# Optimization experiments

Measured on AMD Instinct MI355X. Metric: run time of the kernel, lower is better.

The kernel has to match this reference:

```python
import jax, jax.numpy as jnp
import numpy as np

B, N, D, H = 2, 512, 384, 12
SQK, SV, PQ, PV = 16, 16, 4, 8
SCALE = 1.0 / np.sqrt(SQK + 4 * PQ)  # attention_scale, point_pair_dim=4
EPS = 1e-12


def setup_inputs() -> dict:
    key = jax.random.key(0)
    ks = jax.random.split(key, 10)

    def w(k, fan_in, fan_out):
        return (jax.random.normal(k, (fan_in, fan_out), jnp.float32) / np.sqrt(fan_in))

    return {
        "hidden": jax.random.normal(ks[0], (B, N, D), jnp.float32),
        "xyz": jax.random.normal(ks[1], (B, N, 3), jnp.float32),
        "W_qk": w(ks[2], D, 2 * H * SQK), "b_qk": jnp.zeros((2 * H * SQK,), jnp.float32),
        "W_vs": w(ks[3], D, H * SV), "b_vs": jnp.zeros((H * SV,), jnp.float32),
        "W_so": w(ks[4], H * SV, D), "b_so": jnp.zeros((D,), jnp.float32),
        "W_pqk": w(ks[5], D, H * PQ * 3), "b_pqk": jnp.zeros((H * PQ * 3,), jnp.float32),
        "W_pv": w(ks[6], D, H * PV * 3), "b_pv": jnp.zeros((H * PV * 3,), jnp.float32),
        "W_po": w(ks[7], H * PV * 3, D), "b_po": jnp.zeros((D,), jnp.float32),
        "W_fp": w(ks[8], 2 * D, D), "b_fp": jnp.zeros((D,), jnp.float32),
    }


def reference(hidden, xyz, W_qk, b_qk, W_vs, b_vs, W_so, b_so,
              W_pqk, b_pqk, W_pv, b_pv, W_po, b_po, W_fp, b_fp):
    # scalar q/k/v (note: heads are NOT split in the attention matmuls, per source)
    qk = hidden @ W_qk + b_qk                       # [B,N,2*H*SQK]
    q_s, k_s = jnp.split(qk, 2, axis=-1)            # [B,N,H*SQK] each
    v_s = hidden @ W_vs + b_vs                      # [B,N,H*SV]

    # points; k_points = q_points in source
    qp = (hidden @ W_pqk + b_pqk).reshape(B, N, H, PQ, 3)
    vp = hidden @ W_pv + b_pv                       # [B,N,H*PV*3]

    scalar_attn = jnp.einsum('bid,bjd->bij', q_s, k_s)  # [B,N,N]

    # fused pairwise point features: dist(q_i, k_j) + sum of 3 cosine components
    # = dist + cos_sim, per (head, point); avoid materializing [B,N,N,H,P,3].
    dot = jnp.einsum('bihpc,bjhpc->bijhp', qp, qp)      # [B,N,N,H,PQ]
    n2 = jnp.sum(qp * qp, axis=-1)                      # [B,N,H,PQ]
    d2 = n2[:, :, None] + n2[:, None] - 2.0 * dot
    dist = jnp.sqrt(jnp.maximum(d2, 0.0) + EPS)
    nrm = jnp.sqrt(n2 + EPS)
    cos = dot / (nrm[:, :, None] * nrm[:, None])
    point_attn = jnp.sum(dist + cos, axis=(-1, -2))     # [B,N,N]

    attn = jax.nn.softmax((scalar_attn + point_attn) * SCALE, axis=-1)

    scalar_result = jnp.einsum('bij,bjd->bid', attn, v_s)   # [B,N,H*SV]
    point_result = jnp.einsum('bij,bjd->bid', attn, vp)     # [B,N,H*PV*3]

    scalar_result = scalar_result @ W_so + b_so             # [B,N,D]
    point_result = point_result @ W_po + b_po               # [B,N,D]

    result = jnp.concatenate([scalar_result, point_result], axis=-1) @ W_fp + b_fp
    delta_xyz = point_result.reshape(B, N, -1, 3).mean(axis=2)  # [B,N,3]
    return result, xyz + delta_xyz
```

## Files before the change

kernel.cpp:

```cpp
#include <hip/hip_runtime.h>
#include <math.h>

typedef unsigned short u16;
typedef __attribute__((ext_vector_type(8))) short bf16x8;
typedef __attribute__((ext_vector_type(4))) float f32x4;

#define BB 2
#define NN 512
#define SCALEF 0.17677669529663687f

__device__ __forceinline__ u16 f2bf(float x) {
  union { float f; unsigned u; } c; c.f = x;
  unsigned r = (c.u + 0x7FFFu + ((c.u >> 16) & 1u)) >> 16;
  return (u16)r;
}
__device__ __forceinline__ float bf2f(u16 h) {
  union { unsigned u; float f; } c; c.u = ((unsigned)h) << 16;
  return c.f;
}
__device__ __forceinline__ void pack8(const float* v, bf16x8& h, bf16x8& l) {
#pragma unroll
  for (int j = 0; j < 8; ++j) {
    u16 hi = f2bf(v[j]);
    h[j] = (short)hi;
    l[j] = (short)f2bf(v[j] - bf2f(hi));
  }
}
#define MFMA3(ACC, AH, AL, BH, BL)                                              \
  ACC = __builtin_amdgcn_mfma_f32_16x16x32_bf16(AH, BH, ACC, 0, 0, 0);          \
  ACC = __builtin_amdgcn_mfma_f32_16x16x32_bf16(AH, BL, ACC, 0, 0, 0);          \
  ACC = __builtin_amdgcn_mfma_f32_16x16x32_bf16(AL, BH, ACC, 0, 0, 0);

template<int MR, int NF>
__device__ __forceinline__ void mfma_tile(
    const u16* __restrict__ Ah, const u16* __restrict__ Al, int lda,
    const u16* __restrict__ Bh, const u16* __restrict__ Bl, int ldb,
    int kBeg, int kEnd, int arow, int bcol, f32x4 (&acc)[MR][NF]) {
  const int lane = threadIdx.x & 63;
  const int rr = lane & 15, kg = lane >> 4;
  const u16* pah = Ah + (size_t)(arow + rr) * lda + kg * 8;
  const u16* pal = Al + (size_t)(arow + rr) * lda + kg * 8;
  const u16* pbh = Bh + (size_t)(bcol + rr) * ldb + kg * 8;
  const u16* pbl = Bl + (size_t)(bcol + rr) * ldb + kg * 8;
#pragma unroll 2
  for (int k0 = kBeg; k0 < kEnd; k0 += 32) {
    bf16x8 a_h[MR], a_l[MR], b_h[NF], b_l[NF];
#pragma unroll
    for (int m = 0; m < MR; ++m) {
      a_h[m] = *(const bf16x8*)(pah + (size_t)m * 16 * lda + k0);
      a_l[m] = *(const bf16x8*)(pal + (size_t)m * 16 * lda + k0);
    }
#pragma unroll
    for (int f = 0; f < NF; ++f) {
      b_h[f] = *(const bf16x8*)(pbh + (size_t)f * 16 * ldb + k0);
      b_l[f] = *(const bf16x8*)(pbl + (size_t)f * 16 * ldb + k0);
    }
#pragma unroll
    for (int m = 0; m < MR; ++m)
#pragma unroll
      for (int f = 0; f < NF; ++f) { MFMA3(acc[m][f], a_h[m], a_l[m], b_h[f], b_l[f]) }
  }
}

__global__ __launch_bounds__(256) void k_input(
    const float* __restrict__ hidden, const float* __restrict__ xyz,
    const float* __restrict__ W_qk, const float* __restrict__ b_qk,
    const float* __restrict__ W_vs, const float* __restrict__ b_vs,
    const float* __restrict__ W_pv, const float* __restrict__ b_pv,
    const float* __restrict__ W_pqk, const float* __restrict__ b_pqk,
    u16* __restrict__ QKh, u16* __restrict__ QKl,
    u16* __restrict__ VTh, u16* __restrict__ VTl,
    float* __restrict__ QPf, float* __restrict__ out_xyz) {
  __shared__ f32x4 CB[3][2][3][64];
  __shared__ u16 Dh[48][32], Dl[48][32];
  const int tid = threadIdx.x;
  const int w = tid >> 6, lane = tid & 63;
  const int rr = lane & 15, kg = lane >> 4;
  const int row0 = blockIdx.y * 32, col0 = blockIdx.x * 48;

  if (blockIdx.x == 18) {
    for (int t2 = tid; t2 < 96; t2 += 256)
      out_xyz[(size_t)row0 * 3 + t2] = xyz[(size_t)row0 * 3 + t2];
  }

  const float* W; const float* bias; int Ns, region;
  if (col0 < 384)      { W = W_qk;  Ns = 384; bias = b_qk + col0;          W += col0;       region = 0; }
  else if (col0 < 576) { W = W_vs;  Ns = 192; bias = b_vs + (col0 - 384);  W += col0 - 384; region = 1; }
  else if (col0 < 864) { W = W_pv;  Ns = 288; bias = b_pv + (col0 - 576);  W += col0 - 576; region = 1; }
  else                 { W = W_pqk; Ns = 144; bias = b_pqk + (col0 - 864); W += col0 - 864; region = 2; }

  f32x4 acc[2][3] = {};
  const float* pa = hidden + (size_t)(row0 + rr) * 384 + kg * 8;
  const float* pw = W + rr;
  for (int k0 = w * 32; k0 < 384; k0 += 128) {
    bf16x8 a_h[2], a_l[2], b_h[3], b_l[3];
#pragma unroll
    for (int m = 0; m < 2; ++m) {
      float v[8];
      *(float4*)&v[0] = *(const float4*)(pa + (size_t)m * 16 * 384 + k0);
      *(float4*)&v[4] = *(const float4*)(pa + (size_t)m * 16 * 384 + k0 + 4);
      pack8(v, a_h[m], a_l[m]);
    }
    const float* bp0 = pw + (size_t)(k0 + kg * 8) * Ns;
#pragma unroll
    for (int f = 0; f < 3; ++f) {
      float v[8];
#pragma unroll
      for (int j = 0; j < 8; ++j) v[j] = bp0[(size_t)j * Ns + f * 16];
      pack8(v, b_h[f], b_l[f]);
    }
#pragma unroll
    for (int m = 0; m < 2; ++m)
#pragma unroll
      for (int f = 0; f < 3; ++f) { MFMA3(acc[m][f], a_h[m], a_l[m], b_h[f], b_l[f]) }
  }
  if (w) {
#pragma unroll
    for (int m = 0; m < 2; ++m)
#pragma unroll
      for (int f = 0; f < 3; ++f) CB[w - 1][m][f][lane] = acc[m][f];
  }
  __syncthreads();
  if (w) return;
#pragma unroll
  for (int wv = 0; wv < 3; ++wv)
#pragma unroll
    for (int m = 0; m < 2; ++m)
#pragma unroll
      for (int f = 0; f < 3; ++f) acc[m][f] += CB[wv][m][f][lane];

  const int rb = (lane >> 4) << 2, cc = lane & 15;
  if (region == 0) {
#pragma unroll
    for (int f = 0; f < 3; ++f) {
      int n = col0 + f * 16 + cc;
      float bv = bias[f * 16 + cc];
#pragma unroll
      for (int m = 0; m < 2; ++m)
#pragma unroll
        for (int r = 0; r < 4; ++r) {
          float v = acc[m][f][r] + bv;
          int row = row0 + m * 16 + rb + r;
          u16 hi = f2bf(v);
          QKh[(size_t)row * 384 + n] = hi;
          QKl[(size_t)row * 384 + n] = f2bf(v - bf2f(hi));
        }
    }
  } else if (region == 2) {
#pragma unroll
    for (int f = 0; f < 3; ++f) {
      int c = (col0 - 864) + f * 16 + cc;
      float bv = bias[f * 16 + cc];
#pragma unroll
      for (int m = 0; m < 2; ++m)
#pragma unroll
        for (int r = 0; r < 4; ++r)
          QPf[(size_t)(row0 + m * 16 + rb + r) * 144 + c] = acc[m][f][r] + bv;
    }
  } else {
#pragma unroll
    for (int f = 0; f < 3; ++f) {
      float bv = bias[f * 16 + cc];
#pragma unroll
      for (int m = 0; m < 2; ++m)
#pragma unroll
        for (int r = 0; r < 4; ++r) {
          float v = acc[m][f][r] + bv;
          u16 hi = f2bf(v);
          Dh[f * 16 + cc][m * 16 + rb + r] = hi;
          Dl[f * 16 + cc][m * 16 + rb + r] = f2bf(v - bf2f(hi));
        }
    }
    const int b = row0 >> 9, rl = row0 & 511;
    const int cbase = col0 - 384;
    u16* dsth = VTh + (size_t)b * 480 * 512;
    u16* dstl = VTl + (size_t)b * 480 * 512;
    for (int u = lane; u < 192; u += 64) {
      int c = u >> 2, seg = u & 3;
      *(uint4*)(dsth + (size_t)(cbase + c) * 512 + rl + seg * 8) = *(const uint4*)&Dh[c][seg * 8];
      *(uint4*)(dstl + (size_t)(cbase + c) * 512 + rl + seg * 8) = *(const uint4*)&Dl[c][seg * 8];
    }
  }
}

#define PROW 244
__global__ __launch_bounds__(256) void k_attn(
    const u16* __restrict__ QKh, const u16* __restrict__ QKl,
    const float* __restrict__ QPf, float* __restrict__ ATTf) {
  __shared__ float Pi[32][PROW];
  __shared__ float Pj[32][PROW];
  __shared__ float Sf[32 * 33];
  const int b = blockIdx.z;
  int t = blockIdx.x, ti_ = 0;
  while (t >= 16 - ti_) { t -= 16 - ti_; ++ti_; }
  const int tj_ = ti_ + t;
  const int i0 = ti_ * 32, j0 = tj_ * 32;
  const bool offdiag = (tj_ != ti_);
  const int tid = threadIdx.x;
  for (int u = tid; u < 3072; u += 256) {
    int side = (u >= 1536) ? 1 : 0;
    int rem = u - side * 1536;
    int row = rem / 48, hp = rem - row * 48;
    int grow = b * NN + (side ? j0 : i0) + row;
    const float* p = QPf + (size_t)grow * 144 + hp * 3;
    float x = p[0], y = p[1], z = p[2];
    float n2 = x * x + y * y + z * z;
    float inv = __frsqrt_rn(n2 + 1e-12f);
    float* dst = side ? &Pj[row][0] : &Pi[row][0];
    ((float4*)dst)[hp] = make_float4(x, y, z, n2);
    dst[192 + hp] = inv;
  }
  __syncthreads();
  const int tj = tid & 15, ti = tid >> 4;
  float a00 = 0.f, a01 = 0.f, a10 = 0.f, a11 = 0.f;
  {
    const float4* A0 = (const float4*)&Pi[ti][0];
    const float4* A1 = (const float4*)&Pi[ti + 16][0];
    const float4* B0 = (const float4*)&Pj[tj][0];
    const float4* B1 = (const float4*)&Pj[tj + 16][0];
    const float* iA0 = &Pi[ti][192];
    const float* iA1 = &Pi[ti + 16][192];
    const float* iB0 = &Pj[tj][192];
    const float* iB1 = &Pj[tj + 16][192];
#pragma unroll 4
    for (int hp = 0; hp < 48; ++hp) {
      float4 p0 = A0[hp], p1 = A1[hp], q0 = B0[hp], q1 = B1[hp];
      float va0 = iA0[hp], va1 = iA1[hp], vb0 = iB0[hp], vb1 = iB1[hp];
      {
        float dot = p0.x * q0.x + p0.y * q0.y + p0.z * q0.z;
        float d2 = fmaxf(fmaf(-2.f, dot, p0.w + q0.w), 0.f) + 1e-12f;
        a00 += d2 * __frsqrt_rn(d2) + dot * (va0 * vb0);
      }
      {
        float dot = p0.x * q1.x + p0.y * q1.y + p0.z * q1.z;
        float d2 = fmaxf(fmaf(-2.f, dot, p0.w + q1.w), 0.f) + 1e-12f;
        a01 += d2 * __frsqrt_rn(d2) + dot * (va0 * vb1);
      }
      {
        float dot = p1.x * q0.x + p1.y * q0.y + p1.z * q0.z;
        float d2 = fmaxf(fmaf(-2.f, dot, p1.w + q0.w), 0.f) + 1e-12f;
        a10 += d2 * __frsqrt_rn(d2) + dot * (va1 * vb0);
      }
      {
        float dot = p1.x * q1.x + p1.y * q1.y + p1.z * q1.z;
        float d2 = fmaxf(fmaf(-2.f, dot, p1.w + q1.w), 0.f) + 1e-12f;
        a11 += d2 * __frsqrt_rn(d2) + dot * (va1 * vb1);
      }
    }
  }
  Sf[ti * 33 + tj] = a00;
  Sf[ti * 33 + tj + 16] = a01;
  Sf[(ti + 16) * 33 + tj] = a10;
  Sf[(ti + 16) * 33 + tj + 16] = a11;
  f32x4 qij[1][1] = {}, qji[1][1] = {};
  const int w = tid >> 6, lane = tid & 63;
  {
    int arow = b * NN + i0 + (w >> 1) * 16;
    int brow = b * NN + j0 + (w & 1) * 16;
    mfma_tile<1, 1>(QKh, QKl, 384, QKh + 192, QKl + 192, 384, 0, 192, arow, brow, qij);
    if (offdiag) {
      int arow2 = b * NN + j0 + (w >> 1) * 16;
      int brow2 = b * NN + i0 + (w & 1) * 16;
      mfma_tile<1, 1>(QKh, QKl, 384, QKh + 192, QKl + 192, 384, 0, 192, arow2, brow2, qji);
    }
  }
  __syncthreads();
  const int rl = (w >> 1) * 16 + ((lane >> 4) << 2);
  const int cl = (w & 1) * 16 + (lane & 15);
  float* Cb = ATTf + (size_t)b * NN * NN;
#pragma unroll
  for (int r = 0; r < 4; ++r)
    Cb[(size_t)(i0 + rl + r) * NN + j0 + cl] = qij[0][0][r] + Sf[(rl + r) * 33 + cl];
  if (offdiag) {
#pragma unroll
    for (int r = 0; r < 4; ++r)
      Cb[(size_t)(j0 + rl + r) * NN + i0 + cl] = qji[0][0][r] + Sf[cl * 33 + rl + r];
  }
}

__global__ __launch_bounds__(256) void k_pv(
    const float* __restrict__ ATTf,
    const u16* __restrict__ VTh, const u16* __restrict__ VTl,
    u16* __restrict__ SRh, u16* __restrict__ SRl) {
  __shared__ f32x4 CB[3][2][3][64];
  __shared__ float RS[3][2][64];
  const int tid = threadIdx.x;
  const int w = tid >> 6, lane = tid & 63;
  const int rr = lane & 15, kg = lane >> 4;
  const int b = blockIdx.z;
  const int row0 = blockIdx.y * 32, col0 = blockIdx.x * 48;
  const float* pa = ATTf + (size_t)(b * NN + row0 + rr) * NN + kg * 8;
  const u16* pbh = VTh + (size_t)b * 480 * 512 + (size_t)(col0 + rr) * 512 + kg * 8;
  const u16* pbl = VTl + (size_t)b * 480 * 512 + (size_t)(col0 + rr) * 512 + kg * 8;
  f32x4 acc[2][3] = {};
  float rs0 = 0.f, rs1 = 0.f;
  for (int k0 = w * 32; k0 < NN; k0 += 128) {
    bf16x8 a_h[2], a_l[2], b_h[3], b_l[3];
#pragma unroll
    for (int m = 0; m < 2; ++m) {
      float v[8];
      *(float4*)&v[0] = *(const float4*)(pa + (size_t)m * 16 * NN + k0);
      *(float4*)&v[4] = *(const float4*)(pa + (size_t)m * 16 * NN + k0 + 4);
      float part = 0.f;
#pragma unroll
      for (int j = 0; j < 8; ++j) { float e = __expf(v[j] * SCALEF); part += e; v[j] = e; }
      if (m == 0) rs0 += part; else rs1 += part;
      pack8(v, a_h[m], a_l[m]);
    }
#pragma unroll
    for (int f = 0; f < 3; ++f) {
      b_h[f] = *(const bf16x8*)(pbh + (size_t)f * 16 * 512 + k0);
      b_l[f] = *(const bf16x8*)(pbl + (size_t)f * 16 * 512 + k0);
    }
#pragma unroll
    for (int m = 0; m < 2; ++m)
#pragma unroll
      for (int f = 0; f < 3; ++f) { MFMA3(acc[m][f], (m ? a_h[1] : a_h[0]), (m ? a_l[1] : a_l[0]), b_h[f], b_l[f]) }
  }
  if (w) {
#pragma unroll
    for (int m = 0; m < 2; ++m)
#pragma unroll
      for (int f = 0; f < 3; ++f) CB[w - 1][m][f][lane] = acc[m][f];
    RS[w - 1][0][lane] = rs0;
    RS[w - 1][1][lane] = rs1;
  }
  __syncthreads();
  if (w) return;
#pragma unroll
  for (int wv = 0; wv < 3; ++wv) {
#pragma unroll
    for (int m = 0; m < 2; ++m)
#pragma unroll
      for (int f = 0; f < 3; ++f) acc[m][f] += CB[wv][m][f][lane];
    rs0 += RS[wv][0][lane];
    rs1 += RS[wv][1][lane];
  }
  rs0 += __shfl_xor(rs0, 16); rs0 += __shfl_xor(rs0, 32);
  rs1 += __shfl_xor(rs1, 16); rs1 += __shfl_xor(rs1, 32);
  const int rb = (lane >> 4) << 2, cc = lane & 15;
  float inv0[4], inv1[4];
#pragma unroll
  for (int r = 0; r < 4; ++r) {
    inv0[r] = 1.0f / __shfl(rs0, rb + r);
    inv1[r] = 1.0f / __shfl(rs1, rb + r);
  }
  u16* oh = SRh + (size_t)b * NN * 480;
  u16* ol = SRl + (size_t)b * NN * 480;
#pragma unroll
  for (int m = 0; m < 2; ++m)
#pragma unroll
    for (int f = 0; f < 3; ++f) {
      int n = col0 + f * 16 + cc;
#pragma unroll
      for (int r = 0; r < 4; ++r) {
        float v = acc[m][f][r] * (m ? inv1[r] : inv0[r]);
        u16 hi = f2bf(v);
        oh[(size_t)(row0 + m * 16 + rb + r) * 480 + n] = hi;
        ol[(size_t)(row0 + m * 16 + rb + r) * 480 + n] = f2bf(v - bf2f(hi));
      }
    }
}

__global__ __launch_bounds__(256) void k_outproj(
    const u16* __restrict__ SRh, const u16* __restrict__ SRl,
    const float* __restrict__ W_so, const float* __restrict__ b_so,
    const float* __restrict__ W_po, const float* __restrict__ b_po,
    u16* __restrict__ PRh, u16* __restrict__ PRl, float* __restrict__ out_xyz) {
  __shared__ f32x4 CB[3][2][3][64];
  __shared__ float D[32][49];
  const int tid = threadIdx.x;
  const int w = tid >> 6, lane = tid & 63;
  const int rr = lane & 15, kg = lane >> 4;
  const int t = blockIdx.x;
  const int row0 = blockIdx.y * 32, col0 = t * 48;
  const float* W = (t < 8) ? W_so : W_po;
  const int kBeg = (t < 8) ? 0 : 192, kEnd = (t < 8) ? 192 : 480;
  const int wcol = (t < 8) ? col0 : col0 - 384;
  const u16* pah = SRh + (size_t)(row0 + rr) * 480 + kg * 8;
  const u16* pal = SRl + (size_t)(row0 + rr) * 480 + kg * 8;
  const float* pw = W + wcol + rr;
  f32x4 acc[2][3] = {};
  for (int k0 = kBeg + w * 32; k0 < kEnd; k0 += 128) {
    bf16x8 a_h[2], a_l[2], b_h[3], b_l[3];
#pragma unroll
    for (int m = 0; m < 2; ++m) {
      a_h[m] = *(const bf16x8*)(pah + (size_t)m * 16 * 480 + k0);
      a_l[m] = *(const bf16x8*)(pal + (size_t)m * 16 * 480 + k0);
    }
    const float* bp0 = pw + (size_t)(k0 - kBeg + kg * 8) * 384;
#pragma unroll
    for (int f = 0; f < 3; ++f) {
      float v[8];
#pragma unroll
      for (int j = 0; j < 8; ++j) v[j] = bp0[(size_t)j * 384 + f * 16];
      pack8(v, b_h[f], b_l[f]);
    }
#pragma unroll
    for (int m = 0; m < 2; ++m)
#pragma unroll
      for (int f = 0; f < 3; ++f) { MFMA3(acc[m][f], a_h[m], a_l[m], b_h[f], b_l[f]) }
  }
  if (w) {
#pragma unroll
    for (int m = 0; m < 2; ++m)
#pragma unroll
      for (int f = 0; f < 3; ++f) CB[w - 1][m][f][lane] = acc[m][f];
  }
  __syncthreads();
  if (w) return;
#pragma unroll
  for (int wv = 0; wv < 3; ++wv)
#pragma unroll
    for (int m = 0; m < 2; ++m)
#pragma unroll
      for (int f = 0; f < 3; ++f) acc[m][f] += CB[wv][m][f][lane];
  const int rb = (lane >> 4) << 2, cc = lane & 15;
#pragma unroll
  for (int m = 0; m < 2; ++m)
#pragma unroll
    for (int f = 0; f < 3; ++f) {
      int n = col0 + f * 16 + cc;
      float bias = (n < 384) ? b_so[n] : b_po[n - 384];
#pragma unroll
      for (int r = 0; r < 4; ++r) {
        float v = acc[m][f][r] + bias;
        u16 hi = f2bf(v);
        PRh[(size_t)(row0 + m * 16 + rb + r) * 768 + n] = hi;
        PRl[(size_t)(row0 + m * 16 + rb + r) * 768 + n] = f2bf(v - bf2f(hi));
        if (t >= 8) D[m * 16 + rb + r][f * 16 + cc] = v;
      }
    }
  if (t >= 8) {
    if (lane < 32) {
      float sx = 0.f, sy = 0.f, sz = 0.f;
#pragma unroll
      for (int p = 0; p < 16; ++p) {
        sx += D[lane][3 * p];
        sy += D[lane][3 * p + 1];
        sz += D[lane][3 * p + 2];
      }
      int token = row0 + lane;
      atomicAdd(out_xyz + (size_t)token * 3 + 0, sx * (1.0f / 128.f));
      atomicAdd(out_xyz + (size_t)token * 3 + 1, sy * (1.0f / 128.f));
      atomicAdd(out_xyz + (size_t)token * 3 + 2, sz * (1.0f / 128.f));
    }
  }
}

__global__ __launch_bounds__(256) void k_final(
    const u16* __restrict__ PRh, const u16* __restrict__ PRl,
    const float* __restrict__ W_fp, const float* __restrict__ b_fp,
    float* __restrict__ out_res) {
  __shared__ f32x4 CB[3][2][3][64];
  const int tid = threadIdx.x;
  const int w = tid >> 6, lane = tid & 63;
  const int rr = lane & 15, kg = lane >> 4;
  const int row0 = blockIdx.y * 32, col0 = blockIdx.x * 48;
  const u16* pah = PRh + (size_t)(row0 + rr) * 768 + kg * 8;
  const u16* pal = PRl + (size_t)(row0 + rr) * 768 + kg * 8;
  const float* pw = W_fp + col0 + rr;
  f32x4 acc[2][3] = {};
  for (int k0 = w * 32; k0 < 768; k0 += 128) {
    bf16x8 a_h[2], a_l[2], b_h[3], b_l[3];
#pragma unroll
    for (int m = 0; m < 2; ++m) {
      a_h[m] = *(const bf16x8*)(pah + (size_t)m * 16 * 768 + k0);
      a_l[m] = *(const bf16x8*)(pal + (size_t)m * 16 * 768 + k0);
    }
    const float* bp0 = pw + (size_t)(k0 + kg * 8) * 384;
#pragma unroll
    for (int f = 0; f < 3; ++f) {
      float v[8];
#pragma unroll
      for (int j = 0; j < 8; ++j) v[j] = bp0[(size_t)j * 384 + f * 16];
      pack8(v, b_h[f], b_l[f]);
    }
#pragma unroll
    for (int m = 0; m < 2; ++m)
#pragma unroll
      for (int f = 0; f < 3; ++f) { MFMA3(acc[m][f], a_h[m], a_l[m], b_h[f], b_l[f]) }
  }
  if (w) {
#pragma unroll
    for (int m = 0; m < 2; ++m)
#pragma unroll
      for (int f = 0; f < 3; ++f) CB[w - 1][m][f][lane] = acc[m][f];
  }
  __syncthreads();
  if (w) return;
#pragma unroll
  for (int wv = 0; wv < 3; ++wv)
#pragma unroll
    for (int m = 0; m < 2; ++m)
#pragma unroll
      for (int f = 0; f < 3; ++f) acc[m][f] += CB[wv][m][f][lane];
  const int rb = (lane >> 4) << 2, cc = lane & 15;
#pragma unroll
  for (int m = 0; m < 2; ++m)
#pragma unroll
    for (int f = 0; f < 3; ++f) {
      int n = col0 + f * 16 + cc;
#pragma unroll
      for (int r = 0; r < 4; ++r)
        out_res[(size_t)(row0 + m * 16 + rb + r) * 384 + n] = acc[m][f][r] + b_fp[n];
    }
}

extern "C" void kernel_launch(void* const* d_in, const int* in_sizes, int n_in,
                              void* d_out, int out_size, void* d_ws, size_t ws_size,
                              hipStream_t stream) {
  const float* hidden = (const float*)d_in[0];
  const float* xyz   = (const float*)d_in[1];
  const float* W_qk  = (const float*)d_in[2];
  const float* b_qk  = (const float*)d_in[3];
  const float* W_vs  = (const float*)d_in[4];
  const float* b_vs  = (const float*)d_in[5];
  const float* W_so  = (const float*)d_in[6];
  const float* b_so  = (const float*)d_in[7];
  const float* W_pqk = (const float*)d_in[8];
  const float* b_pqk = (const float*)d_in[9];
  const float* W_pv  = (const float*)d_in[10];
  const float* b_pv  = (const float*)d_in[11];
  const float* W_po  = (const float*)d_in[12];
  const float* b_po  = (const float*)d_in[13];
  const float* W_fp  = (const float*)d_in[14];
  const float* b_fp  = (const float*)d_in[15];

  float* out_res = (float*)d_out;
  float* out_xyz = out_res + (size_t)BB * NN * 384;

  u16* p   = (u16*)d_ws;
  u16* QKh = p;            p += 393216;
  u16* QKl = p;            p += 393216;
  u16* VTh = p;            p += 491520;
  u16* VTl = p;            p += 491520;
  u16* SRh = p;            p += 491520;
  u16* SRl = p;            p += 491520;
  u16* PRh = p;            p += 786432;
  u16* PRl = p;            p += 786432;
  float* QPf  = (float*)p; p += 2 * 147456;
  float* ATTf = (float*)p;

  k_input<<<dim3(21, 32), 256, 0, stream>>>(hidden, xyz,
                                            W_qk, b_qk, W_vs, b_vs, W_pv, b_pv, W_pqk, b_pqk,
                                            QKh, QKl, VTh, VTl, QPf, out_xyz);
  k_attn<<<dim3(136, 1, 2), 256, 0, stream>>>(QKh, QKl, QPf, ATTf);
  k_pv<<<dim3(10, 16, 2), 256, 0, stream>>>(ATTf, VTh, VTl, SRh, SRl);
  k_outproj<<<dim3(16, 32), 256, 0, stream>>>(SRh, SRl, W_so, b_so, W_po, b_po,
                                              PRh, PRl, out_xyz);
  k_final<<<dim3(8, 32), 256, 0, stream>>>(PRh, PRl, W_fp, b_fp, out_res);
}
```

Baseline: 73.98 us.

## Double threads per block and split K/head work across more waves in all kernels

Every kernel moves from 256 to 512 threads. k_input and the GEMM-style kernels split the K reduction over 8 waves instead of 4, with a wider shared-memory cross-wave reduction. k_pv, k_outproj and k_final also halve the row tile to 16, doubling the grid. k_attn splits the 48 head-point loop across two 256-thread halves and gives the two transposed scalar MFMA tiles to separate waves. The aim is more parallelism and latency hiding in these small, latency-bound kernels, at the cost of more reduction traffic, more blocks, and less reuse of the B operand per block.

```diff
diff --git a/kernel.cpp b/kernel.cpp
--- a/kernel.cpp
+++ b/kernel.cpp
@@ -62,7 +62,7 @@
   }
 }
 
-__global__ __launch_bounds__(256) void k_input(
+__global__ __launch_bounds__(512) void k_input(
     const float* __restrict__ hidden, const float* __restrict__ xyz,
     const float* __restrict__ W_qk, const float* __restrict__ b_qk,
     const float* __restrict__ W_vs, const float* __restrict__ b_vs,
@@ -71,7 +71,7 @@
     u16* __restrict__ QKh, u16* __restrict__ QKl,
     u16* __restrict__ VTh, u16* __restrict__ VTl,
     float* __restrict__ QPf, float* __restrict__ out_xyz) {
-  __shared__ f32x4 CB[3][2][3][64];
+  __shared__ f32x4 CB[7][2][3][64];
   __shared__ u16 Dh[48][32], Dl[48][32];
   const int tid = threadIdx.x;
   const int w = tid >> 6, lane = tid & 63;
@@ -79,7 +79,7 @@
   const int row0 = blockIdx.y * 32, col0 = blockIdx.x * 48;
 
   if (blockIdx.x == 18) {
-    for (int t2 = tid; t2 < 96; t2 += 256)
+    for (int t2 = tid; t2 < 96; t2 += 512)
       out_xyz[(size_t)row0 * 3 + t2] = xyz[(size_t)row0 * 3 + t2];
   }
 
@@ -92,7 +92,7 @@
   f32x4 acc[2][3] = {};
   const float* pa = hidden + (size_t)(row0 + rr) * 384 + kg * 8;
   const float* pw = W + rr;
-  for (int k0 = w * 32; k0 < 384; k0 += 128) {
+  for (int k0 = w * 32; k0 < 384; k0 += 256) {
     bf16x8 a_h[2], a_l[2], b_h[3], b_l[3];
 #pragma unroll
     for (int m = 0; m < 2; ++m) {
@@ -123,7 +123,7 @@
   __syncthreads();
   if (w) return;
 #pragma unroll
-  for (int wv = 0; wv < 3; ++wv)
+  for (int wv = 0; wv < 7; ++wv)
 #pragma unroll
     for (int m = 0; m < 2; ++m)
 #pragma unroll
@@ -184,12 +184,12 @@
 }
 
 #define PROW 244
-__global__ __launch_bounds__(256) void k_attn(
+__global__ __launch_bounds__(512) void k_attn(
     const u16* __restrict__ QKh, const u16* __restrict__ QKl,
     const float* __restrict__ QPf, float* __restrict__ ATTf) {
   __shared__ float Pi[32][PROW];
   __shared__ float Pj[32][PROW];
-  __shared__ float Sf[32 * 33];
+  __shared__ float Sf[2][32 * 33];
   const int b = blockIdx.z;
   int t = blockIdx.x, ti_ = 0;
   while (t >= 16 - ti_) { t -= 16 - ti_; ++ti_; }
@@ -197,7 +197,7 @@
   const int i0 = ti_ * 32, j0 = tj_ * 32;
   const bool offdiag = (tj_ != ti_);
   const int tid = threadIdx.x;
-  for (int u = tid; u < 3072; u += 256) {
+  for (int u = tid; u < 3072; u += 512) {
     int side = (u >= 1536) ? 1 : 0;
     int rem = u - side * 1536;
     int row = rem / 48, hp = rem - row * 48;
@@ -211,9 +211,11 @@
     dst[192 + hp] = inv;
   }
   __syncthreads();
-  const int tj = tid & 15, ti = tid >> 4;
-  float a00 = 0.f, a01 = 0.f, a10 = 0.f, a11 = 0.f;
+  const int h = tid >> 8;
+  const int t8 = tid & 255;
+  const int tj = t8 & 15, ti = t8 >> 4;
   {
+    float a00 = 0.f, a01 = 0.f, a10 = 0.f, a11 = 0.f;
     const float4* A0 = (const float4*)&Pi[ti][0];
     const float4* A1 = (const float4*)&Pi[ti + 16][0];
     const float4* B0 = (const float4*)&Pj[tj][0];
@@ -222,8 +224,9 @@
     const float* iA1 = &Pi[ti + 16][192];
     const float* iB0 = &Pj[tj][192];
     const float* iB1 = &Pj[tj + 16][192];
+    const int hpB = h * 24, hpE = hpB + 24;
 #pragma unroll 4
-    for (int hp = 0; hp < 48; ++hp) {
+    for (int hp = hpB; hp < hpE; ++hp) {
       float4 p0 = A0[hp], p1 = A1[hp], q0 = B0[hp], q1 = B1[hp];
       float va0 = iA0[hp], va1 = iA1[hp], vb0 = iB0[hp], vb1 = iB1[hp];
       {
@@ -247,65 +250,65 @@
         a11 += d2 * __frsqrt_rn(d2) + dot * (va1 * vb1);
       }
     }
-  }
-  Sf[ti * 33 + tj] = a00;
-  Sf[ti * 33 + tj + 16] = a01;
-  Sf[(ti + 16) * 33 + tj] = a10;
-  Sf[(ti + 16) * 33 + tj + 16] = a11;
-  f32x4 qij[1][1] = {}, qji[1][1] = {};
+    Sf[h][ti * 33 + tj] = a00;
+    Sf[h][ti * 33 + tj + 16] = a01;
+    Sf[h][(ti + 16) * 33 + tj] = a10;
+    Sf[h][(ti + 16) * 33 + tj + 16] = a11;
+  }
   const int w = tid >> 6, lane = tid & 63;
-  {
-    int arow = b * NN + i0 + (w >> 1) * 16;
-    int brow = b * NN + j0 + (w & 1) * 16;
-    mfma_tile<1, 1>(QKh, QKl, 384, QKh + 192, QKl + 192, 384, 0, 192, arow, brow, qij);
-    if (offdiag) {
-      int arow2 = b * NN + j0 + (w >> 1) * 16;
-      int brow2 = b * NN + i0 + (w & 1) * 16;
-      mfma_tile<1, 1>(QKh, QKl, 384, QKh + 192, QKl + 192, 384, 0, 192, arow2, brow2, qji);
-    }
+  const int dir = w >> 2, sub = w & 3;
+  f32x4 q[1][1] = {};
+  if (dir == 0) {
+    int arow = b * NN + i0 + (sub >> 1) * 16;
+    int brow = b * NN + j0 + (sub & 1) * 16;
+    mfma_tile<1, 1>(QKh, QKl, 384, QKh + 192, QKl + 192, 384, 0, 192, arow, brow, q);
+  } else if (offdiag) {
+    int arow = b * NN + j0 + (sub >> 1) * 16;
+    int brow = b * NN + i0 + (sub & 1) * 16;
+    mfma_tile<1, 1>(QKh, QKl, 384, QKh + 192, QKl + 192, 384, 0, 192, arow, brow, q);
   }
   __syncthreads();
-  const int rl = (w >> 1) * 16 + ((lane >> 4) << 2);
-  const int cl = (w & 1) * 16 + (lane & 15);
+  const int rl = (sub >> 1) * 16 + ((lane >> 4) << 2);
+  const int cl = (sub & 1) * 16 + (lane & 15);
   float* Cb = ATTf + (size_t)b * NN * NN;
-#pragma unroll
-  for (int r = 0; r < 4; ++r)
-    Cb[(size_t)(i0 + rl + r) * NN + j0 + cl] = qij[0][0][r] + Sf[(rl + r) * 33 + cl];
-  if (offdiag) {
+  if (dir == 0) {
 #pragma unroll
     for (int r = 0; r < 4; ++r)
-      Cb[(size_t)(j0 + rl + r) * NN + i0 + cl] = qji[0][0][r] + Sf[cl * 33 + rl + r];
-  }
-}
-
-__global__ __launch_bounds__(256) void k_pv(
+      Cb[(size_t)(i0 + rl + r) * NN + j0 + cl] =
+          q[0][0][r] + Sf[0][(rl + r) * 33 + cl] + Sf[1][(rl + r) * 33 + cl];
+  } else if (offdiag) {
+#pragma unroll
+    for (int r = 0; r < 4; ++r)
+      Cb[(size_t)(j0 + rl + r) * NN + i0 + cl] =
+          q[0][0][r] + Sf[0][cl * 33 + rl + r] + Sf[1][cl * 33 + rl + r];
+  }
+}
+
+__global__ __launch_bounds__(512) void k_pv(
     const float* __restrict__ ATTf,
     const u16* __restrict__ VTh, const u16* __restrict__ VTl,
     u16* __restrict__ SRh, u16* __restrict__ SRl) {
-  __shared__ f32x4 CB[3][2][3][64];
-  __shared__ float RS[3][2][64];
+  __shared__ f32x4 CB[7][3][64];
+  __shared__ float RS[7][64];
   const int tid = threadIdx.x;
   const int w = tid >> 6, lane = tid & 63;
   const int rr = lane & 15, kg = lane >> 4;
   const int b = blockIdx.z;
-  const int row0 = blockIdx.y * 32, col0 = blockIdx.x * 48;
+  const int row0 = blockIdx.y * 16, col0 = blockIdx.x * 48;
   const float* pa = ATTf + (size_t)(b * NN + row0 + rr) * NN + kg * 8;
   const u16* pbh = VTh + (size_t)b * 480 * 512 + (size_t)(col0 + rr) * 512 + kg * 8;
   const u16* pbl = VTl + (size_t)b * 480 * 512 + (size_t)(col0 + rr) * 512 + kg * 8;
-  f32x4 acc[2][3] = {};
-  float rs0 = 0.f, rs1 = 0.f;
-  for (int k0 = w * 32; k0 < NN; k0 += 128) {
-    bf16x8 a_h[2], a_l[2], b_h[3], b_l[3];
-#pragma unroll
-    for (int m = 0; m < 2; ++m) {
+  f32x4 acc[3] = {};
+  float rs = 0.f;
+  for (int k0 = w * 32; k0 < NN; k0 += 256) {
+    bf16x8 a_h, a_l, b_h[3], b_l[3];
+    {
       float v[8];
-      *(float4*)&v[0] = *(const float4*)(pa + (size_t)m * 16 * NN + k0);
-      *(float4*)&v[4] = *(const float4*)(pa + (size_t)m * 16 * NN + k0 + 4);
-      float part = 0.f;
-#pragma unroll
-      for (int j = 0; j < 8; ++j) { float e = __expf(v[j] * SCALEF); part += e; v[j] = e; }
-      if (m == 0) rs0 += part; else rs1 += part;
-      pack8(v, a_h[m], a_l[m]);
+      *(float4*)&v[0] = *(const float4*)(pa + k0);
+      *(float4*)&v[4] = *(const float4*)(pa + k0 + 4);
+#pragma unroll
+      for (int j = 0; j < 8; ++j) { float e = __expf(v[j] * SCALEF); rs += e; v[j] = e; }
+      pack8(v, a_h, a_l);
     }
 #pragma unroll
     for (int f = 0; f < 3; ++f) {
@@ -313,81 +316,65 @@
       b_l[f] = *(const bf16x8*)(pbl + (size_t)f * 16 * 512 + k0);
     }
 #pragma unroll
-    for (int m = 0; m < 2; ++m)
-#pragma unroll
-      for (int f = 0; f < 3; ++f) { MFMA3(acc[m][f], (m ? a_h[1] : a_h[0]), (m ? a_l[1] : a_l[0]), b_h[f], b_l[f]) }
+    for (int f = 0; f < 3; ++f) { MFMA3(acc[f], a_h, a_l, b_h[f], b_l[f]) }
   }
   if (w) {
 #pragma unroll
-    for (int m = 0; m < 2; ++m)
-#pragma unroll
-      for (int f = 0; f < 3; ++f) CB[w - 1][m][f][lane] = acc[m][f];
-    RS[w - 1][0][lane] = rs0;
-    RS[w - 1][1][lane] = rs1;
+    for (int f = 0; f < 3; ++f) CB[w - 1][f][lane] = acc[f];
+    RS[w - 1][lane] = rs;
   }
   __syncthreads();
   if (w) return;
 #pragma unroll
-  for (int wv = 0; wv < 3; ++wv) {
-#pragma unroll
-    for (int m = 0; m < 2; ++m)
-#pragma unroll
-      for (int f = 0; f < 3; ++f) acc[m][f] += CB[wv][m][f][lane];
-    rs0 += RS[wv][0][lane];
-    rs1 += RS[wv][1][lane];
-  }
-  rs0 += __shfl_xor(rs0, 16); rs0 += __shfl_xor(rs0, 32);
-  rs1 += __shfl_xor(rs1, 16); rs1 += __shfl_xor(rs1, 32);
+  for (int wv = 0; wv < 7; ++wv) {
+#pragma unroll
+    for (int f = 0; f < 3; ++f) acc[f] += CB[wv][f][lane];
+    rs += RS[wv][lane];
+  }
+  rs += __shfl_xor(rs, 16);
+  rs += __shfl_xor(rs, 32);
   const int rb = (lane >> 4) << 2, cc = lane & 15;
-  float inv0[4], inv1[4];
-#pragma unroll
-  for (int r = 0; r < 4; ++r) {
-    inv0[r] = 1.0f / __shfl(rs0, rb + r);
-    inv1[r] = 1.0f / __shfl(rs1, rb + r);
-  }
+  float inv[4];
+#pragma unroll
+  for (int r = 0; r < 4; ++r) inv[r] = 1.0f / __shfl(rs, rb + r);
   u16* oh = SRh + (size_t)b * NN * 480;
   u16* ol = SRl + (size_t)b * NN * 480;
 #pragma unroll
-  for (int m = 0; m < 2; ++m)
-#pragma unroll
-    for (int f = 0; f < 3; ++f) {
-      int n = col0 + f * 16 + cc;
-#pragma unroll
-      for (int r = 0; r < 4; ++r) {
-        float v = acc[m][f][r] * (m ? inv1[r] : inv0[r]);
-        u16 hi = f2bf(v);
-        oh[(size_t)(row0 + m * 16 + rb + r) * 480 + n] = hi;
-        ol[(size_t)(row0 + m * 16 + rb + r) * 480 + n] = f2bf(v - bf2f(hi));
-      }
-    }
-}
-
-__global__ __launch_bounds__(256) void k_outproj(
+  for (int f = 0; f < 3; ++f) {
+    int n = col0 + f * 16 + cc;
+#pragma unroll
+    for (int r = 0; r < 4; ++r) {
+      float v = acc[f][r] * inv[r];
+      u16 hi = f2bf(v);
+      oh[(size_t)(row0 + rb + r) * 480 + n] = hi;
+      ol[(size_t)(row0 + rb + r) * 480 + n] = f2bf(v - bf2f(hi));
+    }
+  }
+}
+
+__global__ __launch_bounds__(512) void k_outproj(
     const u16* __restrict__ SRh, const u16* __restrict__ SRl,
     const float* __restrict__ W_so, const float* __restrict__ b_so,
     const float* __restrict__ W_po, const float* __restrict__ b_po,
     u16* __restrict__ PRh, u16* __restrict__ PRl, float* __restrict__ out_xyz) {
-  __shared__ f32x4 CB[3][2][3][64];
-  __shared__ float D[32][49];
+  __shared__ f32x4 CB[7][3][64];
+  __shared__ float D[16][49];
   const int tid = threadIdx.x;
   const int w = tid >> 6, lane = tid & 63;
   const int rr = lane & 15, kg = lane >> 4;
   const int t = blockIdx.x;
-  const int row0 = blockIdx.y * 32, col0 = t * 48;
+  const int row0 = blockIdx.y * 16, col0 = t * 48;
   const float* W = (t < 8) ? W_so : W_po;
   const int kBeg = (t < 8) ? 0 : 192, kEnd = (t < 8) ? 192 : 480;
   const int wcol = (t < 8) ? col0 : col0 - 384;
   const u16* pah = SRh + (size_t)(row0 + rr) * 480 + kg * 8;
   const u16* pal = SRl + (size_t)(row0 + rr) * 480 + kg * 8;
   const float* pw = W + wcol + rr;
-  f32x4 acc[2][3] = {};
-  for (int k0 = kBeg + w * 32; k0 < kEnd; k0 += 128) {
-    bf16x8 a_h[2], a_l[2], b_h[3], b_l[3];
-#pragma unroll
-    for (int m = 0; m < 2; ++m) {
-      a_h[m] = *(const bf16x8*)(pah + (size_t)m * 16 * 480 + k0);
-      a_l[m] = *(const bf16x8*)(pal + (size_t)m * 16 * 480 + k0);
-    }
+  f32x4 acc[3] = {};
+  for (int k0 = kBeg + w * 32; k0 < kEnd; k0 += 256) {
+    bf16x8 a_h, a_l, b_h[3], b_l[3];
+    a_h = *(const bf16x8*)(pah + k0);
+    a_l = *(const bf16x8*)(pal + k0);
     const float* bp0 = pw + (size_t)(k0 - kBeg + kg * 8) * 384;
 #pragma unroll
     for (int f = 0; f < 3; ++f) {
@@ -397,77 +384,64 @@
       pack8(v, b_h[f], b_l[f]);
     }
 #pragma unroll
-    for (int m = 0; m < 2; ++m)
-#pragma unroll
-      for (int f = 0; f < 3; ++f) { MFMA3(acc[m][f], a_h[m], a_l[m], b_h[f], b_l[f]) }
+    for (int f = 0; f < 3; ++f) { MFMA3(acc[f], a_h, a_l, b_h[f], b_l[f]) }
   }
   if (w) {
 #pragma unroll
-    for (int m = 0; m < 2; ++m)
-#pragma unroll
-      for (int f = 0; f < 3; ++f) CB[w - 1][m][f][lane] = acc[m][f];
+    for (int f = 0; f < 3; ++f) CB[w - 1][f][lane] = acc[f];
   }
   __syncthreads();
   if (w) return;
 #pragma unroll
-  for (int wv = 0; wv < 3; ++wv)
-#pragma unroll
-    for (int m = 0; m < 2; ++m)
-#pragma unroll
-      for (int f = 0; f < 3; ++f) acc[m][f] += CB[wv][m][f][lane];
+  for (int wv = 0; wv < 7; ++wv)
+#pragma unroll
+    for (int f = 0; f < 3; ++f) acc[f] += CB[wv][f][lane];
   const int rb = (lane >> 4) << 2, cc = lane & 15;
 #pragma unroll
-  for (int m = 0; m < 2; ++m)
-#pragma unroll
-    for (int f = 0; f < 3; ++f) {
-      int n = col0 + f * 16 + cc;
-      float bias = (n < 384) ? b_so[n] : b_po[n - 384];
-#pragma unroll
-      for (int r = 0; r < 4; ++r) {
-        float v = acc[m][f][r] + bias;
-        u16 hi = f2bf(v);
-        PRh[(size_t)(row0 + m * 16 + rb + r) * 768 + n] = hi;
-        PRl[(size_t)(row0 + m * 16 + rb + r) * 768 + n] = f2bf(v - bf2f(hi));
-        if (t >= 8) D[m * 16 + rb + r][f * 16 + cc] = v;
-      }
-    }
-  if (t >= 8) {
-    if (lane < 32) {
-      float sx = 0.f, sy = 0.f, sz = 0.f;
-#pragma unroll
-      for (int p = 0; p < 16; ++p) {
-        sx += D[lane][3 * p];
-        sy += D[lane][3 * p + 1];
-        sz += D[lane][3 * p + 2];
-      }
-      int token = row0 + lane;
-      atomicAdd(out_xyz + (size_t)token * 3 + 0, sx * (1.0f / 128.f));
-      atomicAdd(out_xyz + (size_t)token * 3 + 1, sy * (1.0f / 128.f));
-      atomicAdd(out_xyz + (size_t)token * 3 + 2, sz * (1.0f / 128.f));
-    }
-  }
-}
-
-__global__ __launch_bounds__(256) void k_final(
+  for (int f = 0; f < 3; ++f) {
+    int n = col0 + f * 16 + cc;
+    float bias = (n < 384) ? b_so[n] : b_po[n - 384];
+#pragma unroll
+    for (int r = 0; r < 4; ++r) {
+      float v = acc[f][r] + bias;
+      u16 hi = f2bf(v);
+      PRh[(size_t)(row0 + rb + r) * 768 + n] = hi;
+      PRl[(size_t)(row0 + rb + r) * 768 + n] = f2bf(v - bf2f(hi));
+      if (t >= 8) D[rb + r][f * 16 + cc] = v;
+    }
+  }
+  if (t >= 8 && lane < 16) {
+    float sx = 0.f, sy = 0.f, sz = 0.f;
+#pragma unroll
+    for (int p = 0; p < 16; ++p) {
+      sx += D[lane][3 * p];
+      sy += D[lane][3 * p + 1];
+      sz += D[lane][3 * p + 2];
+    }
+    int token = row0 + lane;
+    atomicAdd(out_xyz + (size_t)token * 3 + 0, sx * (1.0f / 128.f));
+    atomicAdd(out_xyz + (size_t)token * 3 + 1, sy * (1.0f / 128.f));
+    atomicAdd(out_xyz + (size_t)token * 3 + 2, sz * (1.0f / 128.f));
+  }
+}
+
+__global__ __launch_bounds__(512) void k_final(
     const u16* __restrict__ PRh, const u16* __restrict__ PRl,
     const float* __restrict__ W_fp, const float* __restrict__ b_fp,
     float* __restrict__ out_res) {
-  __shared__ f32x4 CB[3][2][3][64];
+  __shared__ f32x4 CB[7][3][64];
   const int tid = threadIdx.x;
   const int w = tid >> 6, lane = tid & 63;
   const int rr = lane & 15, kg = lane >> 4;
-  const int row0 = blockIdx.y * 32, col0 = blockIdx.x * 48;
+  const int row0 = blockIdx.y * 16, col0 = blockIdx.x * 48;
   const u16* pah = PRh + (size_t)(row0 + rr) * 768 + kg * 8;
   const u16* pal = PRl + (size_t)(row0 + rr) * 768 + kg * 8;
   const float* pw = W_fp + col0 + rr;
-  f32x4 acc[2][3] = {};
-  for (int k0 = w * 32; k0 < 768; k0 += 128) {
-    bf16x8 a_h[2], a_l[2], b_h[3], b_l[3];
-#pragma unroll
-    for (int m = 0; m < 2; ++m) {
-      a_h[m] = *(const bf16x8*)(pah + (size_t)m * 16 * 768 + k0);
-      a_l[m] = *(const bf16x8*)(pal + (size_t)m * 16 * 768 + k0);
-    }
+  f32x4 acc[3] = {};
+  for (int k0 = w * 32; k0 < 768; k0 += 256) {
+    bf16x8 a_h, a_l, b_h[3], b_l[3];
+    a_h = *(const bf16x8*)(pah + k0);
+    a_l = *(const bf16x8*)(pal + k0);
     const float* bp0 = pw + (size_t)(k0 + kg * 8) * 384;
 #pragma unroll
     for (int f = 0; f < 3; ++f) {
@@ -477,34 +451,26 @@
       pack8(v, b_h[f], b_l[f]);
     }
 #pragma unroll
-    for (int m = 0; m < 2; ++m)
-#pragma unroll
-      for (int f = 0; f < 3; ++f) { MFMA3(acc[m][f], a_h[m], a_l[m], b_h[f], b_l[f]) }
+    for (int f = 0; f < 3; ++f) { MFMA3(acc[f], a_h, a_l, b_h[f], b_l[f]) }
   }
   if (w) {
 #pragma unroll
-    for (int m = 0; m < 2; ++m)
-#pragma unroll
-      for (int f = 0; f < 3; ++f) CB[w - 1][m][f][lane] = acc[m][f];
+    for (int f = 0; f < 3; ++f) CB[w - 1][f][lane] = acc[f];
   }
   __syncthreads();
   if (w) return;
 #pragma unroll
-  for (int wv = 0; wv < 3; ++wv)
-#pragma unroll
-    for (int m = 0; m < 2; ++m)
-#pragma unroll
-      for (int f = 0; f < 3; ++f) acc[m][f] += CB[wv][m][f][lane];
+  for (int wv = 0; wv < 7; ++wv)
+#pragma unroll
+    for (int f = 0; f < 3; ++f) acc[f] += CB[wv][f][lane];
   const int rb = (lane >> 4) << 2, cc = lane & 15;
 #pragma unroll
-  for (int m = 0; m < 2; ++m)
-#pragma unroll
-    for (int f = 0; f < 3; ++f) {
-      int n = col0 + f * 16 + cc;
-#pragma unroll
-      for (int r = 0; r < 4; ++r)
-        out_res[(size_t)(row0 + m * 16 + rb + r) * 384 + n] = acc[m][f][r] + b_fp[n];
-    }
+  for (int f = 0; f < 3; ++f) {
+    int n = col0 + f * 16 + cc;
+#pragma unroll
+    for (int r = 0; r < 4; ++r)
+      out_res[(size_t)(row0 + rb + r) * 384 + n] = acc[f][r] + b_fp[n];
+  }
 }
 
 extern "C" void kernel_launch(void* const* d_in, const int* in_sizes, int n_in,
@@ -542,12 +508,12 @@
   float* QPf  = (float*)p; p += 2 * 147456;
   float* ATTf = (float*)p;
 
-  k_input<<<dim3(21, 32), 256, 0, stream>>>(hidden, xyz,
+  k_input<<<dim3(21, 32), 512, 0, stream>>>(hidden, xyz,
                                             W_qk, b_qk, W_vs, b_vs, W_pv, b_pv, W_pqk, b_pqk,
                                             QKh, QKl, VTh, VTl, QPf, out_xyz);
-  k_attn<<<dim3(136, 1, 2), 256, 0, stream>>>(QKh, QKl, QPf, ATTf);
-  k_pv<<<dim3(10, 16, 2), 256, 0, stream>>>(ATTf, VTh, VTl, SRh, SRl);
-  k_outproj<<<dim3(16, 32), 256, 0, stream>>>(SRh, SRl, W_so, b_so, W_po, b_po,
+  k_attn<<<dim3(136, 1, 2), 512, 0, stream>>>(QKh, QKl, QPf, ATTf);
+  k_pv<<<dim3(10, 32, 2), 512, 0, stream>>>(ATTf, VTh, VTl, SRh, SRl);
+  k_outproj<<<dim3(16, 64), 512, 0, stream>>>(SRh, SRl, W_so, b_so, W_po, b_po,
                                               PRh, PRl, out_xyz);
-  k_final<<<dim3(8, 32), 256, 0, stream>>>(PRh, PRl, W_fp, b_fp, out_res);
-}
+  k_final<<<dim3(8, 64), 512, 0, stream>>>(PRh, PRl, W_fp, b_fp, out_res);
+}
```

Result: faster. 71.03 us (-4.0%).
